# Kernel optimization log

Hardware: AMD Instinct MI355X
Metric: run time of the kernel (lower is better)

## Reference

```python
import jax, jax.numpy as jnp
import numpy as np

N_NODES = 100000
N_EDGES = 150000
D_IN = 512
D_HID = 512
N_GRAPHS = 64


def setup_inputs() -> dict:
    key = jax.random.key(0)
    ks = jax.random.split(key, 12)
    x = jax.random.normal(ks[0], (N_NODES, D_IN), dtype=jnp.float32)
    edge_index = jax.random.randint(ks[1], (2, N_EDGES), 0, N_NODES, dtype=jnp.int64)
    batch = jnp.sort(jax.random.randint(ks[2], (N_NODES,), 0, N_GRAPHS, dtype=jnp.int64))
    s1 = 1.0 / np.sqrt(D_IN)
    s2 = 1.0 / np.sqrt(D_HID)
    # GINConv layer 1: MLP([D_IN, D_HID, D_HID])
    W1a = jax.random.uniform(ks[3], (D_IN, D_HID), jnp.float32, -s1, s1)
    b1a = jax.random.uniform(ks[4], (D_HID,), jnp.float32, -s1, s1)
    W1b = jax.random.uniform(ks[5], (D_HID, D_HID), jnp.float32, -s2, s2)
    b1b = jax.random.uniform(ks[6], (D_HID,), jnp.float32, -s2, s2)
    # GINConv layer 2 (out_channels=1): MLP([D_HID, 1, 1])
    W2a = jax.random.uniform(ks[7], (D_HID, 1), jnp.float32, -s2, s2)
    b2a = jax.random.uniform(ks[8], (1,), jnp.float32, -s2, s2)
    W2b = jax.random.uniform(ks[9], (1, 1), jnp.float32, -1.0, 1.0)
    b2b = jax.random.uniform(ks[10], (1,), jnp.float32, -1.0, 1.0)
    return {"x": x, "edge_index": edge_index, "batch": batch,
            "W1a": W1a, "b1a": b1a, "W1b": W1b, "b1b": b1b,
            "W2a": W2a, "b2a": b2a, "W2b": W2b, "b2b": b2b}


def _gin_conv(h, src, dst, Wa, ba, Wb, bb):
    # sum-aggregate neighbor features, add (1+eps)*x with eps=0, then MLP
    agg = jax.ops.segment_sum(h[src], dst, num_segments=N_NODES)  # [N, d]
    z = agg + h
    z = jnp.maximum(jnp.dot(z, Wa) + ba, 0.0)  # Linear -> ReLU
    return jnp.dot(z, Wb) + bb                  # Linear (plain last)


def reference(x, edge_index, batch, W1a, b1a, W1b, b1b, W2a, b2a, W2b, b2b):
    src, dst = edge_index[0], edge_index[1]
    h = _gin_conv(x, src, dst, W1a, b1a, W1b, b1b)
    h = jnp.maximum(h, 0.0)  # inter-layer activation (not applied after last layer)
    h = _gin_conv(h, src, dst, W2a, b2a, W2b, b2b)  # [N, 1]
    # global mean pool over graph assignment
    sums = jax.ops.segment_sum(h, batch, num_segments=N_GRAPHS)  # [G, 1]
    cnt = jax.ops.segment_sum(jnp.ones((N_NODES, 1), h.dtype), batch, num_segments=N_GRAPHS)
    return sums / jnp.maximum(cnt, 1.0)
```

## Files before the change

### kernel.cpp

```cpp
#include <hip/hip_runtime.h>
#include <hip/hip_bf16.h>

#define N_NODES_C 100000
#define N_EDGES_C 150000
#define DC 512
#define NG 64

typedef float f32x4 __attribute__((ext_vector_type(4)));
typedef short s16x8 __attribute__((ext_vector_type(8)));
typedef unsigned int u32;

__device__ __forceinline__ short f2bf(float f) {
    union { float f; unsigned u; } c; c.f = f;
    unsigned r = c.u + 0x7fffu + ((c.u >> 16) & 1u);
    return (short)(r >> 16);
}
__device__ __forceinline__ float bf2f(short v) {
    union { unsigned u; float f; } c;
    c.u = ((unsigned)(unsigned short)v) << 16;
    return c.f;
}

__device__ __forceinline__ void gload16(const void* g, void* l) {
    __builtin_amdgcn_global_load_lds((const __attribute__((address_space(1))) u32*)g,
                                     (__attribute__((address_space(3))) u32*)l,
                                     16, 0, 0);
}


__global__ void zero_k(float* s, float* aggs, int* cnt, float* gsum, float* gcnt) {
    int i = blockIdx.x * 256 + threadIdx.x;
    if (i < N_NODES_C) { s[i] = 0.f; aggs[i] = 0.f; cnt[i] = 0; }
    if (i < NG) { gsum[i] = 0.f; gcnt[i] = 0.f; }
}

__global__ void transpose_w2(const float* __restrict__ in0, const float* __restrict__ in1,
                             short* __restrict__ out0, short* __restrict__ out1) {
    __shared__ float tile[32][33];
    const float* in = blockIdx.z ? in1 : in0;
    short* out = blockIdx.z ? out1 : out0;
    int tx = threadIdx.x & 31;
    int ty = threadIdx.x >> 5;
    int k0 = blockIdx.y * 32;
    int n0 = blockIdx.x * 32;
#pragma unroll
    for (int i = 0; i < 4; ++i)
        tile[ty + i * 8][tx] = in[(size_t)(k0 + ty + i * 8) * DC + n0 + tx];
    __syncthreads();
#pragma unroll
    for (int i = 0; i < 4; ++i)
        out[(size_t)(n0 + ty + i * 8) * DC + k0 + tx] = f2bf(tile[tx][ty + i * 8]);
}


__global__ void hist_k(const int* __restrict__ ei, int* __restrict__ cnt) {
    int e = blockIdx.x * 256 + threadIdx.x;
    if (e < N_EDGES_C) atomicAdd(&cnt[ei[N_EDGES_C + e]], 1);
}

__global__ void scan1_k(const int* __restrict__ cnt, int* __restrict__ off,
                        int* __restrict__ bsum) {
    __shared__ int sh[1024];
    int tid = threadIdx.x;
    int i = blockIdx.x * 1024 + tid;
    int v = (i < N_NODES_C) ? cnt[i] : 0;
    sh[tid] = v;
    __syncthreads();
    for (int d = 1; d < 1024; d <<= 1) {
        int t = (tid >= d) ? sh[tid - d] : 0;
        __syncthreads();
        sh[tid] += t;
        __syncthreads();
    }
    if (i < N_NODES_C) off[i] = sh[tid] - v;
    if (tid == 1023) bsum[blockIdx.x] = sh[1023];
}

#define NSCAN_BLK 98

__global__ void scan2_k(int* __restrict__ bsum) {
    __shared__ int sh[128];
    int tid = threadIdx.x;
    int v = (tid < NSCAN_BLK) ? bsum[tid] : 0;
    sh[tid] = v;
    __syncthreads();
    for (int d = 1; d < 128; d <<= 1) {
        int t = (tid >= d) ? sh[tid - d] : 0;
        __syncthreads();
        sh[tid] += t;
        __syncthreads();
    }
    if (tid < NSCAN_BLK) bsum[tid] = sh[tid] - v;
}

__global__ void scan3_k(int* __restrict__ off, const int* __restrict__ bsum) {
    int i = blockIdx.x * 1024 + threadIdx.x;
    if (i < N_NODES_C) off[i] += bsum[blockIdx.x];
}

__global__ void place_k(const int* __restrict__ ei, int* __restrict__ off,
                        int* __restrict__ ssrc) {
    int e = blockIdx.x * 256 + threadIdx.x;
    if (e < N_EDGES_C) {
        int d = ei[N_EDGES_C + e];
        int p = atomicAdd(&off[d], 1);
        ssrc[p] = ei[e];
    }
}

__global__ void gather_relu_k(const short* __restrict__ y, const int* __restrict__ off,
                              const int* __restrict__ ssrc, const float* __restrict__ b1a,
                              short* __restrict__ z1) {
    int node = blockIdx.x * 4 + (threadIdx.x >> 6);
    if (node >= N_NODES_C) return;
    int t = threadIdx.x & 63;
    const int col = t * 8;
    int beg = (node == 0) ? 0 : off[node - 1];
    int end = off[node];
    s16x8 own = *(const s16x8*)(y + (size_t)node * DC + col);
    float acc[8];
#pragma unroll
    for (int q = 0; q < 8; ++q) acc[q] = bf2f(own[q]);
    int j = beg;
    for (; j + 2 <= end; j += 2) {
        int s0 = ssrc[j];
        int s1 = ssrc[j + 1];
        s16x8 r0 = *(const s16x8*)(y + (size_t)s0 * DC + col);
        s16x8 r1 = *(const s16x8*)(y + (size_t)s1 * DC + col);
#pragma unroll
        for (int q = 0; q < 8; ++q) acc[q] += bf2f(r0[q]) + bf2f(r1[q]);
    }
    if (j < end) {
        int s0 = ssrc[j];
        s16x8 r0 = *(const s16x8*)(y + (size_t)s0 * DC + col);
#pragma unroll
        for (int q = 0; q < 8; ++q) acc[q] += bf2f(r0[q]);
    }
    f32x4 bv0 = *(const f32x4*)(b1a + col);
    f32x4 bv1 = *(const f32x4*)(b1a + col + 4);
    s16x8 o;
    o[0] = f2bf(fmaxf(acc[0] + bv0.x, 0.f));
    o[1] = f2bf(fmaxf(acc[1] + bv0.y, 0.f));
    o[2] = f2bf(fmaxf(acc[2] + bv0.z, 0.f));
    o[3] = f2bf(fmaxf(acc[3] + bv0.w, 0.f));
    o[4] = f2bf(fmaxf(acc[4] + bv1.x, 0.f));
    o[5] = f2bf(fmaxf(acc[5] + bv1.y, 0.f));
    o[6] = f2bf(fmaxf(acc[6] + bv1.z, 0.f));
    o[7] = f2bf(fmaxf(acc[7] + bv1.w, 0.f));
    *(s16x8*)(z1 + (size_t)node * DC + col) = o;
}


__global__ void edge_scalar(const int* __restrict__ ei, const float* __restrict__ s,
                            float* __restrict__ aggs) {
    int e = blockIdx.x * 256 + threadIdx.x;
    if (e < N_EDGES_C) atomicAdd(&aggs[ei[N_EDGES_C + e]], s[ei[e]]);
}

__global__ void node_pool(const float* __restrict__ s, const float* __restrict__ aggs,
                          const int* __restrict__ batch, const float* __restrict__ b2a,
                          float* __restrict__ gsum, float* __restrict__ gcnt) {
    __shared__ float ls[NG], lc[NG];
    int t = threadIdx.x;
    if (t < NG) { ls[t] = 0.f; lc[t] = 0.f; }
    __syncthreads();
    int i = blockIdx.x * 256 + t;
    if (i < N_NODES_C) {
        float z2 = fmaxf(aggs[i] + s[i] + b2a[0], 0.0f);
        int g = batch[i];
        atomicAdd(&ls[g], z2);
        atomicAdd(&lc[g], 1.0f);
    }
    __syncthreads();
    if (t < NG && lc[t] != 0.f) {
        atomicAdd(&gsum[t], ls[t]);
        atomicAdd(&gcnt[t], lc[t]);
    }
}

__global__ void finalize_k(const float* gsum, const float* gcnt, const float* w2b,
                           const float* b2b, float* out) {
    int g = threadIdx.x;
    if (g < NG) {
        float c = fmaxf(gcnt[g], 1.0f);
        out[g] = gsum[g] / c * w2b[0] + b2b[0];
    }
}

#define BM 128
#define BN 128
#define BK 32
#define NKT (DC / BK)
#define NWG 3128
#define WPX 391

__global__ __launch_bounds__(256, 3) void gemm0_k(const float* __restrict__ Ap,
                                                  const short* __restrict__ Bt,
                                                  short* __restrict__ Cout) {
    __shared__ alignas(16) short As[BM * BK];
    __shared__ alignas(16) short Bs[BN * BK];

    const int tid = threadIdx.x;
    const int bid = blockIdx.x;
    const int lin = (bid & 7) * WPX + (bid >> 3);
    const int brow = (lin >> 2) * BM;
    const int bcol = (lin & 3) * BN;

    const int w    = tid >> 6;
    const int lane = tid & 63;
    const int wr   = (w >> 1) * 64;
    const int wc   = (w & 1) * 64;
    const int lr   = lane & 15;
    const int lg   = lane >> 4;
    const int lswz = (lr >> 1) & 3;

    f32x4 acc[4][4] = {};

    const int srow = lane >> 2;
    const int scol = (((lane & 3) ^ ((srow >> 1) & 3)) * 8);

    const short* bg0 = Bt + (size_t)(bcol + w * 32 + srow) * DC + scol;
    const short* bg1 = bg0 + (size_t)16 * DC;
    short* bl0 = &Bs[(w * 32) * BK];
    short* bl1 = &Bs[(w * 32 + 16) * BK];

    const int rAl = tid >> 1;
    int r = brow + rAl;
    if (r >= N_NODES_C) r = N_NODES_C - 1;
    const float* axsrc = Ap + (size_t)r * DC + (tid & 1) * 16;
    const int rswz = (rAl >> 1) & 3;
    const int awoff0 = rAl * BK + ((((tid & 1) * 2 + 0) ^ rswz) * 8);
    const int awoff1 = rAl * BK + ((((tid & 1) * 2 + 1) ^ rswz) * 8);

    f32x4 areg[4];
#pragma unroll
    for (int q = 0; q < 4; ++q) areg[q] = *(const f32x4*)(axsrc + q * 4);

    for (int kt = 0; kt < NKT; ++kt) {
        const int k0 = kt * BK;
        __syncthreads();
        s16x8 c0, c1;
        c0[0] = f2bf(areg[0].x); c0[1] = f2bf(areg[0].y);
        c0[2] = f2bf(areg[0].z); c0[3] = f2bf(areg[0].w);
        c0[4] = f2bf(areg[1].x); c0[5] = f2bf(areg[1].y);
        c0[6] = f2bf(areg[1].z); c0[7] = f2bf(areg[1].w);
        c1[0] = f2bf(areg[2].x); c1[1] = f2bf(areg[2].y);
        c1[2] = f2bf(areg[2].z); c1[3] = f2bf(areg[2].w);
        c1[4] = f2bf(areg[3].x); c1[5] = f2bf(areg[3].y);
        c1[6] = f2bf(areg[3].z); c1[7] = f2bf(areg[3].w);
        *(s16x8*)&As[awoff0] = c0;
        *(s16x8*)&As[awoff1] = c1;
        gload16(bg0 + k0, bl0);
        gload16(bg1 + k0, bl1);
        __syncthreads();

        if (kt + 1 < NKT) {
#pragma unroll
            for (int q = 0; q < 4; ++q)
                areg[q] = *(const f32x4*)(axsrc + (kt + 1) * BK + q * 4);
        }

        s16x8 af[4], bfr[4];
#pragma unroll
        for (int mi = 0; mi < 4; ++mi)
            af[mi] = *(const s16x8*)&As[(wr + mi * 16 + lr) * BK + ((lg ^ lswz) * 8)];
#pragma unroll
        for (int ni = 0; ni < 4; ++ni)
            bfr[ni] = *(const s16x8*)&Bs[(wc + ni * 16 + lr) * BK + ((lg ^ lswz) * 8)];
        __builtin_amdgcn_s_setprio(1);
#pragma unroll
        for (int mi = 0; mi < 4; ++mi)
#pragma unroll
            for (int ni = 0; ni < 4; ++ni)
                acc[mi][ni] = __builtin_amdgcn_mfma_f32_16x16x32_bf16(af[mi], bfr[ni],
                                                                      acc[mi][ni], 0, 0, 0);
        __builtin_amdgcn_s_setprio(0);
    }

    const int rb = brow + wr + lg * 4;
    const int cb = bcol + wc + lr;
#pragma unroll
    for (int mi = 0; mi < 4; ++mi) {
#pragma unroll
        for (int rr = 0; rr < 4; ++rr) {
            int row = rb + mi * 16 + rr;
            if (row < N_NODES_C) {
#pragma unroll
                for (int ni = 0; ni < 4; ++ni)
                    Cout[(size_t)row * DC + cb + ni * 16] = f2bf(acc[mi][ni][rr]);
            }
        }
    }
}

#define G2_BM 256
#define G2_NWG 1564

__global__ __launch_bounds__(512, 2) void gemm1_k(const short* __restrict__ A,
                                                  const short* __restrict__ Bt,
                                                  const float* __restrict__ bias,
                                                  const float* __restrict__ w2a,
                                                  float* __restrict__ s_out) {
    __shared__ alignas(16) short As[G2_BM * BK];
    __shared__ alignas(16) short Bs[BN * BK];

    const int tid = threadIdx.x;
    const int bid = blockIdx.x;
    const int q = G2_NWG / 8, rr8 = G2_NWG % 8;
    const int xcd = bid & 7;
    const int lin = (xcd < rr8 ? xcd * (q + 1) : rr8 * (q + 1) + (xcd - rr8) * q) + (bid >> 3);
    const int brow = (lin >> 2) * G2_BM;
    const int bcol = (lin & 3) * BN;

    const int w    = tid >> 6;
    const int lane = tid & 63;
    const int wm   = w >> 1;
    const int wn   = w & 1;
    const int lr   = lane & 15;
    const int lg   = lane >> 4;
    const int lswz = (lr >> 1) & 3;

    f32x4 acc[4][4] = {};

    const int srow = lane >> 2;
    const int scol = (((lane & 3) ^ ((srow >> 1) & 3)) * 8);

    int ar0 = brow + w * 32 + srow;
    int ar1 = ar0 + 16;
    if (ar0 >= N_NODES_C) ar0 = N_NODES_C - 1;
    if (ar1 >= N_NODES_C) ar1 = N_NODES_C - 1;
    const short* ag0 = A + (size_t)ar0 * DC + scol;
    const short* ag1 = A + (size_t)ar1 * DC + scol;
    short* al0 = &As[(w * 32) * BK];
    short* al1 = &As[(w * 32 + 16) * BK];
    const short* bg = Bt + (size_t)(bcol + w * 16 + srow) * DC + scol;
    short* bl = &Bs[(w * 16) * BK];

    for (int kt = 0; kt < NKT; ++kt) {
        const int k0 = kt * BK;
        __syncthreads();
        gload16(ag0 + k0, al0);
        gload16(ag1 + k0, al1);
        gload16(bg + k0, bl);
        __syncthreads();

        s16x8 af[4], bfr[4];
#pragma unroll
        for (int mi = 0; mi < 4; ++mi)
            af[mi] = *(const s16x8*)&As[(wm * 64 + mi * 16 + lr) * BK + ((lg ^ lswz) * 8)];
#pragma unroll
        for (int ni = 0; ni < 4; ++ni)
            bfr[ni] = *(const s16x8*)&Bs[(wn * 64 + ni * 16 + lr) * BK + ((lg ^ lswz) * 8)];
        __builtin_amdgcn_s_setprio(1);
#pragma unroll
        for (int mi = 0; mi < 4; ++mi)
#pragma unroll
            for (int ni = 0; ni < 4; ++ni)
                acc[mi][ni] = __builtin_amdgcn_mfma_f32_16x16x32_bf16(af[mi], bfr[ni],
                                                                      acc[mi][ni], 0, 0, 0);
        __builtin_amdgcn_s_setprio(0);
    }

    const int rb = brow + wm * 64 + lg * 4;
    const int cb = bcol + wn * 64 + lr;

    float bv[4], wv[4];
#pragma unroll
    for (int ni = 0; ni < 4; ++ni) {
        bv[ni] = bias[cb + ni * 16];
        wv[ni] = w2a[cb + ni * 16];
    }
#pragma unroll
    for (int mi = 0; mi < 4; ++mi) {
#pragma unroll
        for (int rr = 0; rr < 4; ++rr) {
            float sum = 0.f;
#pragma unroll
            for (int ni = 0; ni < 4; ++ni) {
                float v = fmaxf(acc[mi][ni][rr] + bv[ni], 0.0f);
                sum += v * wv[ni];
            }
#pragma unroll
            for (int off = 1; off < 16; off <<= 1) sum += __shfl_xor(sum, off, 64);
            int row = rb + mi * 16 + rr;
            if (lr == 0 && row < N_NODES_C) atomicAdd(&s_out[row], sum);
        }
    }
}


extern "C" void kernel_launch(void* const* d_in, const int* in_sizes, int n_in,
                              void* d_out, int out_size, void* d_ws, size_t ws_size,
                              hipStream_t stream) {
    const float* x     = (const float*)d_in[0];
    const int*   ei    = (const int*)d_in[1];
    const int*   batch = (const int*)d_in[2];
    const float* W1a   = (const float*)d_in[3];
    const float* b1a   = (const float*)d_in[4];
    const float* W1b   = (const float*)d_in[5];
    const float* b1b   = (const float*)d_in[6];
    const float* W2a   = (const float*)d_in[7];
    const float* b2a   = (const float*)d_in[8];
    const float* W2b   = (const float*)d_in[9];
    const float* b2b   = (const float*)d_in[10];
    float* out = (float*)d_out;

    char* w = (char*)d_ws;
    short* z1   = (short*)(w);
    short* y    = (short*)(w + 102400000);
    short* WT1  = (short*)(w + 204800000);
    short* WT2  = (short*)(w + 205324288);
    float* sbuf = (float*)(w + 205848576);
    float* aggs = (float*)(w + 206248576);
    int*   cnt  = (int*)  (w + 206648576);
    int*   offb = (int*)  (w + 207048576);
    int*   ssrc = (int*)  (w + 207448576);
    int*   bsum = (int*)  (w + 208048576);
    float* gsum = (float*)(w + 208049088);
    float* gcnt = (float*)(w + 208049344);

    zero_k<<<391, 256, 0, stream>>>(sbuf, aggs, cnt, gsum, gcnt);
    transpose_w2<<<dim3(16, 16, 2), 256, 0, stream>>>(W1a, W1b, WT1, WT2);

    hist_k<<<586, 256, 0, stream>>>(ei, cnt);
    scan1_k<<<NSCAN_BLK, 1024, 0, stream>>>(cnt, offb, bsum);
    scan2_k<<<1, 128, 0, stream>>>(bsum);
    scan3_k<<<NSCAN_BLK, 1024, 0, stream>>>(offb, bsum);
    place_k<<<586, 256, 0, stream>>>(ei, offb, ssrc);

    gemm0_k<<<NWG, 256, 0, stream>>>(x, WT1, y);
    gather_relu_k<<<25000, 256, 0, stream>>>(y, offb, ssrc, b1a, z1);
    gemm1_k<<<G2_NWG, 512, 0, stream>>>(z1, WT2, b1b, W2a, sbuf);

    edge_scalar<<<586, 256, 0, stream>>>(ei, sbuf, aggs);
    node_pool<<<391, 256, 0, stream>>>(sbuf, aggs, batch, b2a, gsum, gcnt);
    finalize_k<<<1, 64, 0, stream>>>(gsum, gcnt, W2b, b2b, out);
}
```

Before: 299.5 us.

## Revert gemm1 to 128-row tiles, drop setprio, replace zero kernel with memsets

The second GEMM goes back from 256-row tiles with 512 threads to the smaller 128-row tile shape with 256 threads, the same as the first GEMM, including its XCD mapping. The s_setprio hints around the MFMA loops are removed in both GEMMs. The zeroing kernel is replaced by two hipMemsetAsync calls covering the contiguous scalar buffers and the pooling accumulators. Smaller tiles load more B per output but allow more blocks per CU, and the memsets drop one kernel launch.

```diff
diff --git a/kernel.cpp b/kernel.cpp
--- a/kernel.cpp
+++ b/kernel.cpp
@@ -27,12 +27,6 @@
                                      16, 0, 0);
 }
 
-
-__global__ void zero_k(float* s, float* aggs, int* cnt, float* gsum, float* gcnt) {
-    int i = blockIdx.x * 256 + threadIdx.x;
-    if (i < N_NODES_C) { s[i] = 0.f; aggs[i] = 0.f; cnt[i] = 0; }
-    if (i < NG) { gsum[i] = 0.f; gcnt[i] = 0.f; }
-}
 
 __global__ void transpose_w2(const float* __restrict__ in0, const float* __restrict__ in1,
                              short* __restrict__ out0, short* __restrict__ out1) {
@@ -267,14 +261,12 @@
 #pragma unroll
         for (int ni = 0; ni < 4; ++ni)
             bfr[ni] = *(const s16x8*)&Bs[(wc + ni * 16 + lr) * BK + ((lg ^ lswz) * 8)];
-        __builtin_amdgcn_s_setprio(1);
 #pragma unroll
         for (int mi = 0; mi < 4; ++mi)
 #pragma unroll
             for (int ni = 0; ni < 4; ++ni)
                 acc[mi][ni] = __builtin_amdgcn_mfma_f32_16x16x32_bf16(af[mi], bfr[ni],
                                                                       acc[mi][ni], 0, 0, 0);
-        __builtin_amdgcn_s_setprio(0);
     }
 
     const int rb = brow + wr + lg * 4;
@@ -293,29 +285,24 @@
     }
 }
 
-#define G2_BM 256
-#define G2_NWG 1564
-
-__global__ __launch_bounds__(512, 2) void gemm1_k(const short* __restrict__ A,
+__global__ __launch_bounds__(256, 4) void gemm1_k(const short* __restrict__ A,
                                                   const short* __restrict__ Bt,
                                                   const float* __restrict__ bias,
                                                   const float* __restrict__ w2a,
                                                   float* __restrict__ s_out) {
-    __shared__ alignas(16) short As[G2_BM * BK];
+    __shared__ alignas(16) short As[BM * BK];
     __shared__ alignas(16) short Bs[BN * BK];
 
     const int tid = threadIdx.x;
     const int bid = blockIdx.x;
-    const int q = G2_NWG / 8, rr8 = G2_NWG % 8;
-    const int xcd = bid & 7;
-    const int lin = (xcd < rr8 ? xcd * (q + 1) : rr8 * (q + 1) + (xcd - rr8) * q) + (bid >> 3);
-    const int brow = (lin >> 2) * G2_BM;
+    const int lin = (bid & 7) * WPX + (bid >> 3);
+    const int brow = (lin >> 2) * BM;
     const int bcol = (lin & 3) * BN;
 
     const int w    = tid >> 6;
     const int lane = tid & 63;
-    const int wm   = w >> 1;
-    const int wn   = w & 1;
+    const int wr   = (w >> 1) * 64;
+    const int wc   = (w & 1) * 64;
     const int lr   = lane & 15;
     const int lg   = lane >> 4;
     const int lswz = (lr >> 1) & 3;
@@ -333,36 +320,37 @@
     const short* ag1 = A + (size_t)ar1 * DC + scol;
     short* al0 = &As[(w * 32) * BK];
     short* al1 = &As[(w * 32 + 16) * BK];
-    const short* bg = Bt + (size_t)(bcol + w * 16 + srow) * DC + scol;
-    short* bl = &Bs[(w * 16) * BK];
+    const short* bg0 = Bt + (size_t)(bcol + w * 32 + srow) * DC + scol;
+    const short* bg1 = bg0 + (size_t)16 * DC;
+    short* bl0 = &Bs[(w * 32) * BK];
+    short* bl1 = &Bs[(w * 32 + 16) * BK];
 
     for (int kt = 0; kt < NKT; ++kt) {
         const int k0 = kt * BK;
         __syncthreads();
         gload16(ag0 + k0, al0);
         gload16(ag1 + k0, al1);
-        gload16(bg + k0, bl);
+        gload16(bg0 + k0, bl0);
+        gload16(bg1 + k0, bl1);
         __syncthreads();
 
         s16x8 af[4], bfr[4];
 #pragma unroll
         for (int mi = 0; mi < 4; ++mi)
-            af[mi] = *(const s16x8*)&As[(wm * 64 + mi * 16 + lr) * BK + ((lg ^ lswz) * 8)];
+            af[mi] = *(const s16x8*)&As[(wr + mi * 16 + lr) * BK + ((lg ^ lswz) * 8)];
 #pragma unroll
         for (int ni = 0; ni < 4; ++ni)
-            bfr[ni] = *(const s16x8*)&Bs[(wn * 64 + ni * 16 + lr) * BK + ((lg ^ lswz) * 8)];
-        __builtin_amdgcn_s_setprio(1);
+            bfr[ni] = *(const s16x8*)&Bs[(wc + ni * 16 + lr) * BK + ((lg ^ lswz) * 8)];
 #pragma unroll
         for (int mi = 0; mi < 4; ++mi)
 #pragma unroll
             for (int ni = 0; ni < 4; ++ni)
                 acc[mi][ni] = __builtin_amdgcn_mfma_f32_16x16x32_bf16(af[mi], bfr[ni],
                                                                       acc[mi][ni], 0, 0, 0);
-        __builtin_amdgcn_s_setprio(0);
-    }
-
-    const int rb = brow + wm * 64 + lg * 4;
-    const int cb = bcol + wn * 64 + lr;
+    }
+
+    const int rb = brow + wr + lg * 4;
+    const int cb = bcol + wc + lr;
 
     float bv[4], wv[4];
 #pragma unroll
@@ -419,7 +407,8 @@
     float* gsum = (float*)(w + 208049088);
     float* gcnt = (float*)(w + 208049344);
 
-    zero_k<<<391, 256, 0, stream>>>(sbuf, aggs, cnt, gsum, gcnt);
+    hipMemsetAsync(sbuf, 0, 1200000, stream);
+    hipMemsetAsync(gsum, 0, 512, stream);
     transpose_w2<<<dim3(16, 16, 2), 256, 0, stream>>>(W1a, W1b, WT1, WT2);
 
     hist_k<<<586, 256, 0, stream>>>(ei, cnt);
@@ -430,7 +419,7 @@
 
     gemm0_k<<<NWG, 256, 0, stream>>>(x, WT1, y);
     gather_relu_k<<<25000, 256, 0, stream>>>(y, offb, ssrc, b1a, z1);
-    gemm1_k<<<G2_NWG, 512, 0, stream>>>(z1, WT2, b1b, W2a, sbuf);
+    gemm1_k<<<NWG, 256, 0, stream>>>(z1, WT2, b1b, W2a, sbuf);
 
     edge_scalar<<<586, 256, 0, stream>>>(ei, sbuf, aggs);
     node_pool<<<391, 256, 0, stream>>>(sbuf, aggs, batch, b2a, gsum, gcnt);
```

Result: no change. 304.6 us (+1.7%).
